# Kernel tuning notes

Measured on AMD Instinct MI355X. Metric: run time of the kernel, lower is better.

The kernel has to match this reference:

```python
import jax, jax.numpy as jnp
import numpy as np
import itertools

L, F, T = 16, 2, 2**19          # levels, features/level, hashmap size
BASE, SCALE = 16, 1.5           # base resolution, per-level scale
N = 524288                      # batch of sample points
PRIMES = np.array([1, 2654435761, 805459861, 3674653429], dtype=np.uint32)


def hash_encode(x, table):
    """Multi-resolution hash-grid encoding. x: [N,d] in [0,1); table: [L,T,F]."""
    n, d = x.shape
    corners = jnp.asarray(list(itertools.product([0, 1], repeat=d)), dtype=jnp.uint32)  # [C,d]
    primes = jnp.asarray(PRIMES[:d])
    is_hi = corners.astype(bool)[None]          # [1,C,d]
    outs = []
    for l in range(L):
        res = float(np.floor(BASE * SCALE**l))
        pos = x * res
        p0f = jnp.floor(pos)
        frac = pos - p0f                         # [N,d]
        p0 = p0f.astype(jnp.uint32)
        coords = p0[:, None, :] + corners[None]  # [N,C,d] uint32 (wraps)
        m = coords * primes                      # [N,C,d]
        h = m[..., 0]
        for j in range(1, d):
            h = h ^ m[..., j]
        idx = (h % np.uint32(T)).astype(jnp.int32)              # [N,C]
        w = jnp.where(is_hi, frac[:, None, :], 1.0 - frac[:, None, :]).prod(-1)  # [N,C]
        feat = table[l][idx]                                    # [N,C,F]
        outs.append(jnp.einsum('nc,ncf->nf', w, feat))
    return jnp.concatenate(outs, axis=-1)        # [N, L*F]


def mlp(h, w_in, w_hid, w_out):
    """tcnn-style bias-free MLP, ReLU hidden, linear output."""
    h = jax.nn.relu(h @ w_in)
    for i in range(w_hid.shape[0]):
        h = jax.nn.relu(h @ w_hid[i])
    return h @ w_out


def setup_inputs() -> dict:
    key = jax.random.key(0)
    ks = jax.random.split(key, 20)
    def w(k, shape):
        fan = shape[-2]
        return jax.random.normal(k, shape, jnp.float32) / np.sqrt(fan).astype(np.float32)
    return {
        'x': jax.random.uniform(ks[0], (N, 3), jnp.float32),
        't': jax.random.uniform(ks[1], (1,), jnp.float32),
        'skip_alpha': jax.random.uniform(ks[2], (1,), jnp.float32),
        'table_s': jax.random.normal(ks[3], (L, T, F), jnp.float32) * 1e-2,
        'ws_in': w(ks[4], (32, 64)),
        'ws_hid': w(ks[5], (3, 64, 64)),
        'ws_out': w(ks[6], (64, 64)),
        'table_d': jax.random.normal(ks[7], (L, T, F), jnp.float32) * 1e-2,
        'wd_in': w(ks[8], (32, 64)),
        'wd_hid': w(ks[9], (3, 64, 64)),
        'wd_out': w(ks[10], (64, 64)),
        'w1_in': w(ks[11], (128, 64)),
        'w1_hid': w(ks[12], (1, 64, 64)),
        'w1_out': w(ks[13], (64, 128)),
        'w2_in': w(ks[14], (128, 64)),
        'w2_hid': w(ks[15], (1, 64, 64)),
        'w2_out': w(ks[16], (64, 1)),
    }


def reference(x, t, skip_alpha, table_s, ws_in, ws_hid, ws_out,
              table_d, wd_in, wd_hid, wd_out,
              w1_in, w1_hid, w1_out, w2_in, w2_hid, w2_out):
    static_features = mlp(hash_encode(x, table_s), ws_in, ws_hid, ws_out)          # [N,64]
    t_col = jnp.broadcast_to(t, (x.shape[0], 1))
    x4 = jnp.concatenate([x, t_col], axis=1)                                        # [N,4]
    dynamic_features = mlp(hash_encode(x4, table_d), wd_in, wd_hid, wd_out)        # [N,64]
    features = jnp.concatenate([static_features, dynamic_features], axis=-1)       # [N,128]
    out1 = mlp(features, w1_in, w1_hid, w1_out)                                     # [N,128]
    blended = out1 * skip_alpha + (1.0 - skip_alpha) * features
    return mlp(blended, w2_in, w2_hid, w2_out)                                      # [N,1]
```

## Files before the change

### kernel.cpp

```cpp
#include <hip/hip_runtime.h>
#include <hip/hip_bf16.h>
#include <stdint.h>

#define LVLS 16
#define TSZ  524288
#define TMASK 0x7FFFFu
#define NPTS 524288
#define P1 2654435761u
#define P2 805459861u
#define P3 3674653429u

__constant__ float RES_TAB[16] = {
    16.f, 24.f, 36.f, 54.f, 81.f, 121.f, 182.f, 273.f,
    410.f, 615.f, 922.f, 1383.f, 2075.f, 3113.f, 4670.f, 7006.f};

using f16x8 = __attribute__((ext_vector_type(8))) _Float16;
using f32x4 = __attribute__((ext_vector_type(4))) float;

union PackF16 { uint32_t u; _Float16 h[2]; };

constexpr int PS = 72;

struct WPtrs { const float* p[11]; };

__global__ void k_weights(WPtrs wp, _Float16* __restrict__ dst) {
    int id = blockIdx.x * 256 + threadIdx.x;
    if (id >= 69632) return;
    const int OFF[16] = {0,2048,6144,10240,14336,18432,20480,24576,28672,
                         32768,36864,45056,49152,57344,65536,69632};
    const int KK[15]  = {32,64,64,64,64,32,64,64,64,64,128,64,64,128,64};
    const int NN[15]  = {64,64,64,64,64,64,64,64,64,64,64,64,128,64,64};
    const int PSEL[15]= {0,1,1,1,2,3,4,4,4,5,6,7,8,9,10};
    const int POFF[15]= {0,0,4096,8192,0,0,0,4096,8192,0,0,0,0,0,0};
    int m = 0;
    while (id >= OFF[m+1]) m++;
    int local = id - OFF[m];
    int j    = local & 7;
    int lane = (local >> 3) & 63;
    int blk  = local >> 9;
    int KC   = KK[m] >> 5;
    int ct   = blk / KC;
    int kc   = blk - ct * KC;
    int k    = kc*32 + ((lane>>4)<<3) + j;
    int n    = ct*16 + (lane & 15);
    const float* src = wp.p[PSEL[m]] + POFF[m];
    dst[id] = (_Float16)src[k * NN[m] + n];
}

__global__ void k_tables(const float* __restrict__ ts, const float* __restrict__ td,
                         const float* __restrict__ tptr, uint2* __restrict__ Tc) {
    int id = blockIdx.x * 256 + threadIdx.x;
    int l = id >> 19, i = id & TMASK;
    float2 sv = ((const float2*)ts)[id];
    float res = RES_TAB[l];
    float tv  = tptr[0];
    float pt  = tv * res;
    float fpt = floorf(pt);
    float ft  = pt - fpt;
    uint32_t ut = (uint32_t)(int)fpt;
    uint32_t h0 = (ut * P3) & TMASK;
    uint32_t h1 = ((ut + 1u) * P3) & TMASK;
    const float2* tdl = (const float2*)td + (size_t)l * TSZ;
    float2 a = tdl[i ^ h0];
    float2 b = tdl[i ^ h1];
    PackF16 o0, o1;
    o0.h[0] = (_Float16)sv.x; o0.h[1] = (_Float16)sv.y;
    o1.h[0] = (_Float16)((1.f - ft) * a.x + ft * b.x);
    o1.h[1] = (_Float16)((1.f - ft) * a.y + ft * b.y);
    Tc[id] = make_uint2(o0.u, o1.u);
}

__device__ __forceinline__ void enc_batch4(const float* __restrict__ x,
                                           const uint2* __restrict__ tcl, float res,
                                           uint32_t* __restrict__ es,
                                           uint32_t* __restrict__ ed, int pb) {
    float fr[4][3];
    uint2 v[4][8];
#pragma unroll
    for (int b = 0; b < 4; b++) {
        int p = pb + b * 65536;
        float px = x[p*3+0]*res, py = x[p*3+1]*res, pz = x[p*3+2]*res;
        float fx = floorf(px), fy = floorf(py), fz = floorf(pz);
        fr[b][0] = px-fx; fr[b][1] = py-fy; fr[b][2] = pz-fz;
        uint32_t ux = (uint32_t)(int)fx, uy = (uint32_t)(int)fy, uz = (uint32_t)(int)fz;
        uint32_t hx[2] = {ux, ux + 1u};
        uint32_t hy[2] = {uy * P1, (uy + 1u) * P1};
        uint32_t hz[2] = {uz * P2, (uz + 1u) * P2};
#pragma unroll
        for (int c = 0; c < 8; c++) {
            uint32_t idx = (hx[c&1] ^ hy[(c>>1)&1] ^ hz[c>>2]) & TMASK;
            v[b][c] = tcl[idx];
        }
    }
#pragma unroll
    for (int b = 0; b < 4; b++) {
        float wxa[2] = {1.f - fr[b][0], fr[b][0]};
        float wya[2] = {1.f - fr[b][1], fr[b][1]};
        float wza[2] = {1.f - fr[b][2], fr[b][2]};
        float sA0 = 0.f, sA1 = 0.f, sD0 = 0.f, sD1 = 0.f;
#pragma unroll
        for (int c = 0; c < 8; c++) {
            float w = wxa[c&1] * wya[(c>>1)&1] * wza[c>>2];
            PackF16 s, d; s.u = v[b][c].x; d.u = v[b][c].y;
            sA0 += w * (float)s.h[0]; sA1 += w * (float)s.h[1];
            sD0 += w * (float)d.h[0]; sD1 += w * (float)d.h[1];
        }
        PackF16 o;
        int p = pb + b * 65536;
        o.h[0] = (_Float16)sA0; o.h[1] = (_Float16)sA1; es[p] = o.u;
        o.h[0] = (_Float16)sD0; o.h[1] = (_Float16)sD1; ed[p] = o.u;
    }
}

__launch_bounds__(256, 4)
__global__ void k_encode(const float* __restrict__ x,
                         const uint2* __restrict__ Tc,
                         uint32_t* __restrict__ EncS, uint32_t* __restrict__ EncD) {
    int tid = threadIdx.x;
    int cls = blockIdx.x & 7;
    int gt  = (blockIdx.x >> 3) * 256 + tid;
#pragma unroll
    for (int u3 = 0; u3 < 3; u3++) {
        int u = cls * 3 + u3;
        int l = 4 + (u >> 1);
        int pb = (u & 1) * 262144 + gt;
        enc_batch4(x, Tc + (size_t)l * TSZ, RES_TAB[l],
                   EncS + (size_t)l * NPTS, EncD + (size_t)l * NPTS, pb);
    }
    {
        int l = cls >> 1;
        int pb = (cls & 1) * 262144 + gt;
        enc_batch4(x, Tc + (size_t)l * TSZ, RES_TAB[l],
                   EncS + (size_t)l * NPTS, EncD + (size_t)l * NPTS, pb);
    }
}

__device__ __forceinline__ void wait_lds() {
    asm volatile("s_waitcnt lgkmcnt(0)" ::: "memory");
}

template<int KC, bool RELU>
__device__ __forceinline__ void mm2(const f16x8 a[2][4], const f16x8* __restrict__ B,
                                    _Float16* dst, int m, int quad, int lane) {
#pragma unroll
    for (int ct = 0; ct < 4; ct++) {
        f32x4 acc0 = {0.f,0.f,0.f,0.f}, acc1 = {0.f,0.f,0.f,0.f};
#pragma unroll
        for (int kc = 0; kc < KC; kc++) {
            f16x8 b = B[(ct*KC+kc)*64 + lane];
            acc0 = __builtin_amdgcn_mfma_f32_16x16x32_f16(a[0][kc], b, acc0, 0, 0, 0);
            acc1 = __builtin_amdgcn_mfma_f32_16x16x32_f16(a[1][kc], b, acc1, 0, 0, 0);
        }
#pragma unroll
        for (int i = 0; i < 4; i++) {
            float v0 = acc0[i], v1 = acc1[i];
            if (RELU) { v0 = fmaxf(v0, 0.f); v1 = fmaxf(v1, 0.f); }
            dst[(0*16 + quad*4+i)*PS + ct*16 + m] = (_Float16)v0;
            dst[(1*16 + quad*4+i)*PS + ct*16 + m] = (_Float16)v1;
        }
    }
}

template<int KC>
__device__ __forceinline__ void mm2_keep(const f16x8 a[2][4], const f16x8* __restrict__ B,
                                         _Float16* dst, PackF16 P[2][8],
                                         int m, int quad, int lane) {
#pragma unroll
    for (int ct = 0; ct < 4; ct++) {
        f32x4 acc0 = {0.f,0.f,0.f,0.f}, acc1 = {0.f,0.f,0.f,0.f};
#pragma unroll
        for (int kc = 0; kc < KC; kc++) {
            f16x8 b = B[(ct*KC+kc)*64 + lane];
            acc0 = __builtin_amdgcn_mfma_f32_16x16x32_f16(a[0][kc], b, acc0, 0, 0, 0);
            acc1 = __builtin_amdgcn_mfma_f32_16x16x32_f16(a[1][kc], b, acc1, 0, 0, 0);
        }
#pragma unroll
        for (int ih = 0; ih < 2; ih++) {
            PackF16 p0, p1;
            p0.h[0] = (_Float16)acc0[ih*2+0]; p0.h[1] = (_Float16)acc0[ih*2+1];
            p1.h[0] = (_Float16)acc1[ih*2+0]; p1.h[1] = (_Float16)acc1[ih*2+1];
            P[0][ct*2+ih] = p0; P[1][ct*2+ih] = p1;
            dst[(0*16 + quad*4+ih*2+0)*PS + ct*16 + m] = p0.h[0];
            dst[(0*16 + quad*4+ih*2+1)*PS + ct*16 + m] = p0.h[1];
            dst[(1*16 + quad*4+ih*2+0)*PS + ct*16 + m] = p1.h[0];
            dst[(1*16 + quad*4+ih*2+1)*PS + ct*16 + m] = p1.h[1];
        }
    }
}

template<int KC>
__device__ __forceinline__ void read_a(const _Float16* buf, f16x8 a[2][4], int m, int quad) {
#pragma unroll
    for (int rt = 0; rt < 2; rt++)
#pragma unroll
        for (int kc = 0; kc < KC; kc++)
            a[rt][kc] = *(const f16x8*)(buf + (rt*16 + m)*PS + kc*32 + quad*8);
}

__device__ __forceinline__ void read_a128(const _Float16* Fs, const _Float16* Fd,
                                          f16x8 a[2][4], int m, int quad) {
#pragma unroll
    for (int rt = 0; rt < 2; rt++) {
#pragma unroll
        for (int kc = 0; kc < 2; kc++) {
            a[rt][kc]   = *(const f16x8*)(Fs + (rt*16 + m)*PS + kc*32 + quad*8);
            a[rt][kc+2] = *(const f16x8*)(Fd + (rt*16 + m)*PS + kc*32 + quad*8);
        }
    }
}

__device__ __forceinline__ void load_enc(const uint32_t* __restrict__ Enc,
                                         int pbase, int m, int quad, f16x8 a[2][4]) {
#pragma unroll
    for (int rt = 0; rt < 2; rt++) {
        union { uint32_t u[4]; f16x8 v; } cv;
        int p = pbase + rt*16 + m;
#pragma unroll
        for (int j = 0; j < 4; j++)
            cv.u[j] = Enc[(size_t)(quad*4 + j) * NPTS + p];
        a[rt][0] = cv.v;
    }
}

__launch_bounds__(256, 4)
__global__ void k_mlp(const uint32_t* __restrict__ EncS, const uint32_t* __restrict__ EncD,
                      const _Float16* __restrict__ Wfrag, const float* __restrict__ alphap,
                      const float* __restrict__ w2out, float* __restrict__ out) {
    __shared__ _Float16 FsB[4][32*PS];
    __shared__ _Float16 FdB[4][32*PS];
    int tid  = threadIdx.x;
    int wave = tid >> 6, lane = tid & 63;
    int m = lane & 15, quad = lane >> 4;
    int pbase = blockIdx.x * 128 + wave * 32;
    _Float16* Fs = FsB[wave];
    _Float16* Fd = FdB[wave];
    const f16x8* W8 = (const f16x8*)Wfrag;
    float alpha = alphap[0];

    f16x8 a[2][4];
    PackF16 sP[2][8], dP[2][8];

    load_enc(EncS, pbase, m, quad, a);
    mm2<1, true>(a, W8 + 0,    Fs, m, quad, lane); wait_lds();
    read_a<2>(Fs, a, m, quad);
    mm2<2, true>(a, W8 + 256,  Fs, m, quad, lane); wait_lds();
    read_a<2>(Fs, a, m, quad);
    mm2<2, true>(a, W8 + 768,  Fs, m, quad, lane); wait_lds();
    read_a<2>(Fs, a, m, quad);
    mm2<2, true>(a, W8 + 1280, Fs, m, quad, lane); wait_lds();
    read_a<2>(Fs, a, m, quad);
    mm2_keep<2>(a, W8 + 1792, Fs, sP, m, quad, lane);
    load_enc(EncD, pbase, m, quad, a);
    mm2<1, true>(a, W8 + 2304, Fd, m, quad, lane); wait_lds();
    read_a<2>(Fd, a, m, quad);
    mm2<2, true>(a, W8 + 2560, Fd, m, quad, lane); wait_lds();
    read_a<2>(Fd, a, m, quad);
    mm2<2, true>(a, W8 + 3072, Fd, m, quad, lane); wait_lds();
    read_a<2>(Fd, a, m, quad);
    mm2<2, true>(a, W8 + 3584, Fd, m, quad, lane); wait_lds();
    read_a<2>(Fd, a, m, quad);
    mm2_keep<2>(a, W8 + 4096, Fd, dP, m, quad, lane); wait_lds();
    read_a128(Fs, Fd, a, m, quad);
    mm2<4, true>(a, W8 + 4608, Fs, m, quad, lane); wait_lds();
    read_a<2>(Fs, a, m, quad);
    mm2<2, true>(a, W8 + 5632, Fs, m, quad, lane); wait_lds();
    read_a<2>(Fs, a, m, quad);
#pragma unroll
    for (int ct = 0; ct < 8; ct++) {
        f32x4 acc0 = {0.f,0.f,0.f,0.f}, acc1 = {0.f,0.f,0.f,0.f};
#pragma unroll
        for (int kc = 0; kc < 2; kc++) {
            f16x8 b = W8[6144 + (ct*2+kc)*64 + lane];
            acc0 = __builtin_amdgcn_mfma_f32_16x16x32_f16(a[0][kc], b, acc0, 0, 0, 0);
            acc1 = __builtin_amdgcn_mfma_f32_16x16x32_f16(a[1][kc], b, acc1, 0, 0, 0);
        }
        _Float16* tgt = (ct < 4) ? Fs : Fd;
        int col = (ct & 3) * 16 + m;
#pragma unroll
        for (int i = 0; i < 4; i++) {
            float f0 = (ct < 4) ? (float)sP[0][ct*2 + (i>>1)].h[i&1]
                                : (float)dP[0][(ct-4)*2 + (i>>1)].h[i&1];
            float f1 = (ct < 4) ? (float)sP[1][ct*2 + (i>>1)].h[i&1]
                                : (float)dP[1][(ct-4)*2 + (i>>1)].h[i&1];
            tgt[(0*16 + quad*4+i)*PS + col] = (_Float16)(alpha*acc0[i] + (1.f-alpha)*f0);
            tgt[(1*16 + quad*4+i)*PS + col] = (_Float16)(alpha*acc1[i] + (1.f-alpha)*f1);
        }
    }
    wait_lds();
    read_a128(Fs, Fd, a, m, quad);
    mm2<4, true>(a, W8 + 7168, Fs, m, quad, lane); wait_lds();
    read_a<2>(Fs, a, m, quad);
    float rsum0[4] = {0.f,0.f,0.f,0.f}, rsum1[4] = {0.f,0.f,0.f,0.f};
#pragma unroll
    for (int ct = 0; ct < 4; ct++) {
        f32x4 acc0 = {0.f,0.f,0.f,0.f}, acc1 = {0.f,0.f,0.f,0.f};
#pragma unroll
        for (int kc = 0; kc < 2; kc++) {
            f16x8 b = W8[8192 + (ct*2+kc)*64 + lane];
            acc0 = __builtin_amdgcn_mfma_f32_16x16x32_f16(a[0][kc], b, acc0, 0, 0, 0);
            acc1 = __builtin_amdgcn_mfma_f32_16x16x32_f16(a[1][kc], b, acc1, 0, 0, 0);
        }
        float wv = w2out[ct*16 + m];
#pragma unroll
        for (int i = 0; i < 4; i++) {
            rsum0[i] += fmaxf(acc0[i], 0.f) * wv;
            rsum1[i] += fmaxf(acc1[i], 0.f) * wv;
        }
    }
#pragma unroll
    for (int off = 1; off < 16; off <<= 1) {
#pragma unroll
        for (int i = 0; i < 4; i++) {
            rsum0[i] += __shfl_xor(rsum0[i], off, 64);
            rsum1[i] += __shfl_xor(rsum1[i], off, 64);
        }
    }
    if (m == 0) {
#pragma unroll
        for (int i = 0; i < 4; i++) {
            out[pbase + 0*16 + quad*4 + i] = rsum0[i];
            out[pbase + 1*16 + quad*4 + i] = rsum1[i];
        }
    }
}

extern "C" void kernel_launch(void* const* d_in, const int* in_sizes, int n_in,
                              void* d_out, int out_size, void* d_ws, size_t ws_size,
                              hipStream_t stream) {
    const float* x      = (const float*)d_in[0];
    const float* t      = (const float*)d_in[1];
    const float* alpha  = (const float*)d_in[2];
    const float* tab_s  = (const float*)d_in[3];
    const float* ws_in  = (const float*)d_in[4];
    const float* ws_hid = (const float*)d_in[5];
    const float* ws_out = (const float*)d_in[6];
    const float* tab_d  = (const float*)d_in[7];
    const float* wd_in  = (const float*)d_in[8];
    const float* wd_hid = (const float*)d_in[9];
    const float* wd_out = (const float*)d_in[10];
    const float* w1_in  = (const float*)d_in[11];
    const float* w1_hid = (const float*)d_in[12];
    const float* w1_out = (const float*)d_in[13];
    const float* w2_in  = (const float*)d_in[14];
    const float* w2_hid = (const float*)d_in[15];
    const float* w2_out = (const float*)d_in[16];
    float* out = (float*)d_out;

    char* ws = (char*)d_ws;
    _Float16* Wfrag = (_Float16*)ws;
    uint2*    Tc    = (uint2*)(ws + 139264);
    uint32_t* EncS  = (uint32_t*)(ws + 139264 + 67108864);
    uint32_t* EncD  = EncS + (size_t)LVLS * NPTS;
    size_t needed = 139264 + 67108864 + 2ull * 33554432ull;
    if (ws_size < needed) return;

    WPtrs wp;
    wp.p[0] = ws_in;  wp.p[1] = ws_hid; wp.p[2] = ws_out;
    wp.p[3] = wd_in;  wp.p[4] = wd_hid; wp.p[5] = wd_out;
    wp.p[6] = w1_in;  wp.p[7] = w1_hid; wp.p[8] = w1_out;
    wp.p[9] = w2_in;  wp.p[10] = w2_hid;

    k_weights<<<272,   256, 0, stream>>>(wp, Wfrag);
    k_tables <<<32768, 256, 0, stream>>>(tab_s, tab_d, t, Tc);
    k_encode <<<2048,  256, 0, stream>>>(x, Tc, EncS, EncD);
    k_mlp    <<<NPTS/128, 256, 0, stream>>>(EncS, EncD, Wfrag, alpha, w2_out, out);
}
```

Before: 619.9 us.

## Fuse weight and table prep kernels; reorder per-level encode schedule

Merges the weight-fragment conversion and the combined hash-table build into one k_build launch. Table blocks are ordered by level groups (0-3, 12-15, 4-11) so the build order roughly matches the order in which k_encode reads levels, with the aim of cache reuse. k_encode now processes one point at a time per level in non-unrolled loops instead of batches of four, and drops the occupancy hint in the launch bounds. The new block mapping rewrites levels 12-15 twice, which adds redundant work. Processing one point at a time also leaves fewer independent gathers in flight per thread.

Result: faster. 597.3 us (-3.6%).

```diff
diff --git a/kernel.cpp b/kernel.cpp
--- a/kernel.cpp
+++ b/kernel.cpp
@@ -23,115 +23,133 @@
 
 struct WPtrs { const float* p[11]; };
 
-__global__ void k_weights(WPtrs wp, _Float16* __restrict__ dst) {
-    int id = blockIdx.x * 256 + threadIdx.x;
-    if (id >= 69632) return;
-    const int OFF[16] = {0,2048,6144,10240,14336,18432,20480,24576,28672,
-                         32768,36864,45056,49152,57344,65536,69632};
-    const int KK[15]  = {32,64,64,64,64,32,64,64,64,64,128,64,64,128,64};
-    const int NN[15]  = {64,64,64,64,64,64,64,64,64,64,64,64,128,64,64};
-    const int PSEL[15]= {0,1,1,1,2,3,4,4,4,5,6,7,8,9,10};
-    const int POFF[15]= {0,0,4096,8192,0,0,0,4096,8192,0,0,0,0,0,0};
-    int m = 0;
-    while (id >= OFF[m+1]) m++;
-    int local = id - OFF[m];
-    int j    = local & 7;
-    int lane = (local >> 3) & 63;
-    int blk  = local >> 9;
-    int KC   = KK[m] >> 5;
-    int ct   = blk / KC;
-    int kc   = blk - ct * KC;
-    int k    = kc*32 + ((lane>>4)<<3) + j;
-    int n    = ct*16 + (lane & 15);
-    const float* src = wp.p[PSEL[m]] + POFF[m];
-    dst[id] = (_Float16)src[k * NN[m] + n];
-}
-
-__global__ void k_tables(const float* __restrict__ ts, const float* __restrict__ td,
-                         const float* __restrict__ tptr, uint2* __restrict__ Tc) {
-    int id = blockIdx.x * 256 + threadIdx.x;
-    int l = id >> 19, i = id & TMASK;
-    float2 sv = ((const float2*)ts)[id];
-    float res = RES_TAB[l];
-    float tv  = tptr[0];
-    float pt  = tv * res;
-    float fpt = floorf(pt);
-    float ft  = pt - fpt;
-    uint32_t ut = (uint32_t)(int)fpt;
-    uint32_t h0 = (ut * P3) & TMASK;
-    uint32_t h1 = ((ut + 1u) * P3) & TMASK;
-    const float2* tdl = (const float2*)td + (size_t)l * TSZ;
-    float2 a = tdl[i ^ h0];
-    float2 b = tdl[i ^ h1];
-    PackF16 o0, o1;
-    o0.h[0] = (_Float16)sv.x; o0.h[1] = (_Float16)sv.y;
-    o1.h[0] = (_Float16)((1.f - ft) * a.x + ft * b.x);
-    o1.h[1] = (_Float16)((1.f - ft) * a.y + ft * b.y);
-    Tc[id] = make_uint2(o0.u, o1.u);
-}
-
-__device__ __forceinline__ void enc_batch4(const float* __restrict__ x,
-                                           const uint2* __restrict__ tcl, float res,
-                                           uint32_t* __restrict__ es,
-                                           uint32_t* __restrict__ ed, int pb) {
-    float fr[4][3];
-    uint2 v[4][8];
-#pragma unroll
-    for (int b = 0; b < 4; b++) {
-        int p = pb + b * 65536;
-        float px = x[p*3+0]*res, py = x[p*3+1]*res, pz = x[p*3+2]*res;
-        float fx = floorf(px), fy = floorf(py), fz = floorf(pz);
-        fr[b][0] = px-fx; fr[b][1] = py-fy; fr[b][2] = pz-fz;
-        uint32_t ux = (uint32_t)(int)fx, uy = (uint32_t)(int)fy, uz = (uint32_t)(int)fz;
-        uint32_t hx[2] = {ux, ux + 1u};
-        uint32_t hy[2] = {uy * P1, (uy + 1u) * P1};
-        uint32_t hz[2] = {uz * P2, (uz + 1u) * P2};
-#pragma unroll
-        for (int c = 0; c < 8; c++) {
-            uint32_t idx = (hx[c&1] ^ hy[(c>>1)&1] ^ hz[c>>2]) & TMASK;
-            v[b][c] = tcl[idx];
-        }
-    }
-#pragma unroll
-    for (int b = 0; b < 4; b++) {
-        float wxa[2] = {1.f - fr[b][0], fr[b][0]};
-        float wya[2] = {1.f - fr[b][1], fr[b][1]};
-        float wza[2] = {1.f - fr[b][2], fr[b][2]};
-        float sA0 = 0.f, sA1 = 0.f, sD0 = 0.f, sD1 = 0.f;
-#pragma unroll
-        for (int c = 0; c < 8; c++) {
-            float w = wxa[c&1] * wya[(c>>1)&1] * wza[c>>2];
-            PackF16 s, d; s.u = v[b][c].x; d.u = v[b][c].y;
-            sA0 += w * (float)s.h[0]; sA1 += w * (float)s.h[1];
-            sD0 += w * (float)d.h[0]; sD1 += w * (float)d.h[1];
-        }
-        PackF16 o;
-        int p = pb + b * 65536;
-        o.h[0] = (_Float16)sA0; o.h[1] = (_Float16)sA1; es[p] = o.u;
-        o.h[0] = (_Float16)sD0; o.h[1] = (_Float16)sD1; ed[p] = o.u;
-    }
-}
-
-__launch_bounds__(256, 4)
+__global__ void k_build(const float* __restrict__ ts, const float* __restrict__ td,
+                        const float* __restrict__ tptr, uint2* __restrict__ Tc,
+                        WPtrs wp, _Float16* __restrict__ wdst) {
+    int B = blockIdx.x;
+    int tid = threadIdx.x;
+    if (B < 40960) {
+        int c = B & 7, j = B >> 3;
+        int l, i;
+        if (j < 1024) {
+            l = c >> 1;
+            i = (c & 1) * 262144 + j * 256 + tid;
+        } else if (j < 3072) {
+            l = 12 + (c >> 1);
+            i = (j - 1024) * 256 + tid;
+        } else {
+            l = 4 + c;
+            i = (j - 3072) * 256 + tid;
+        }
+        int id = l * TSZ + i;
+        float2 sv = ((const float2*)ts)[id];
+        float res = RES_TAB[l];
+        float tv  = tptr[0];
+        float pt  = tv * res;
+        float fpt = floorf(pt);
+        float ft  = pt - fpt;
+        uint32_t ut = (uint32_t)(int)fpt;
+        uint32_t h0 = (ut * P3) & TMASK;
+        uint32_t h1 = ((ut + 1u) * P3) & TMASK;
+        const float2* tdl = (const float2*)td + (size_t)l * TSZ;
+        float2 a = tdl[i ^ h0];
+        float2 b = tdl[i ^ h1];
+        PackF16 o0, o1;
+        o0.h[0] = (_Float16)sv.x; o0.h[1] = (_Float16)sv.y;
+        o1.h[0] = (_Float16)((1.f - ft) * a.x + ft * b.x);
+        o1.h[1] = (_Float16)((1.f - ft) * a.y + ft * b.y);
+        Tc[id] = make_uint2(o0.u, o1.u);
+    } else {
+        int id = (B - 40960) * 256 + tid;
+        if (id >= 69632) return;
+        const int OFF[16] = {0,2048,6144,10240,14336,18432,20480,24576,28672,
+                             32768,36864,45056,49152,57344,65536,69632};
+        const int KK[15]  = {32,64,64,64,64,32,64,64,64,64,128,64,64,128,64};
+        const int NN[15]  = {64,64,64,64,64,64,64,64,64,64,64,64,128,64,64};
+        const int PSEL[15]= {0,1,1,1,2,3,4,4,4,5,6,7,8,9,10};
+        const int POFF[15]= {0,0,4096,8192,0,0,0,4096,8192,0,0,0,0,0,0};
+        int m = 0;
+        while (id >= OFF[m+1]) m++;
+        int local = id - OFF[m];
+        int jj   = local & 7;
+        int lane = (local >> 3) & 63;
+        int blk  = local >> 9;
+        int KC   = KK[m] >> 5;
+        int ct   = blk / KC;
+        int kc   = blk - ct * KC;
+        int k    = kc*32 + ((lane>>4)<<3) + jj;
+        int n    = ct*16 + (lane & 15);
+        const float* src = wp.p[PSEL[m]] + POFF[m];
+        wdst[id] = (_Float16)src[k * NN[m] + n];
+    }
+}
+
+__device__ __forceinline__ void enc_point(const float* __restrict__ x,
+                                          const uint2* __restrict__ tcl, float res,
+                                          uint32_t* __restrict__ es,
+                                          uint32_t* __restrict__ ed, int p) {
+    float px = x[p*3+0]*res, py = x[p*3+1]*res, pz = x[p*3+2]*res;
+    float fx = floorf(px), fy = floorf(py), fz = floorf(pz);
+    float wx = px-fx, wy = py-fy, wz = pz-fz;
+    uint32_t ux = (uint32_t)(int)fx, uy = (uint32_t)(int)fy, uz = (uint32_t)(int)fz;
+    uint32_t hx[2] = {ux, ux + 1u};
+    uint32_t hy[2] = {uy * P1, (uy + 1u) * P1};
+    uint32_t hz[2] = {uz * P2, (uz + 1u) * P2};
+    uint2 v[8];
+#pragma unroll
+    for (int c = 0; c < 8; c++) {
+        uint32_t idx = (hx[c&1] ^ hy[(c>>1)&1] ^ hz[c>>2]) & TMASK;
+        v[c] = tcl[idx];
+    }
+    float wxa[2] = {1.f-wx, wx}, wya[2] = {1.f-wy, wy}, wza[2] = {1.f-wz, wz};
+    float sA0 = 0.f, sA1 = 0.f, sD0 = 0.f, sD1 = 0.f;
+#pragma unroll
+    for (int c = 0; c < 8; c++) {
+        float w = wxa[c&1] * wya[(c>>1)&1] * wza[c>>2];
+        PackF16 s, d; s.u = v[c].x; d.u = v[c].y;
+        sA0 += w * (float)s.h[0]; sA1 += w * (float)s.h[1];
+        sD0 += w * (float)d.h[0]; sD1 += w * (float)d.h[1];
+    }
+    PackF16 o;
+    o.h[0] = (_Float16)sA0; o.h[1] = (_Float16)sA1; es[p] = o.u;
+    o.h[0] = (_Float16)sD0; o.h[1] = (_Float16)sD1; ed[p] = o.u;
+}
+
+__launch_bounds__(256)
 __global__ void k_encode(const float* __restrict__ x,
                          const uint2* __restrict__ Tc,
                          uint32_t* __restrict__ EncS, uint32_t* __restrict__ EncD) {
     int tid = threadIdx.x;
-    int cls = blockIdx.x & 7;
+    int c   = blockIdx.x & 7;
     int gt  = (blockIdx.x >> 3) * 256 + tid;
-#pragma unroll
-    for (int u3 = 0; u3 < 3; u3++) {
-        int u = cls * 3 + u3;
-        int l = 4 + (u >> 1);
-        int pb = (u & 1) * 262144 + gt;
-        enc_batch4(x, Tc + (size_t)l * TSZ, RES_TAB[l],
-                   EncS + (size_t)l * NPTS, EncD + (size_t)l * NPTS, pb);
-    }
     {
-        int l = cls >> 1;
-        int pb = (cls & 1) * 262144 + gt;
-        enc_batch4(x, Tc + (size_t)l * TSZ, RES_TAB[l],
-                   EncS + (size_t)l * NPTS, EncD + (size_t)l * NPTS, pb);
+        int l = 4 + c;
+        const uint2* tcl = Tc + (size_t)l * TSZ;
+        uint32_t* es = EncS + (size_t)l * NPTS;
+        uint32_t* ed = EncD + (size_t)l * NPTS;
+        float res = RES_TAB[l];
+        for (int q = 0; q < 8; q++)
+            enc_point(x, tcl, res, es, ed, gt + q * 65536);
+    }
+    {
+        int l = 12 + (c >> 1);
+        const uint2* tcl = Tc + (size_t)l * TSZ;
+        uint32_t* es = EncS + (size_t)l * NPTS;
+        uint32_t* ed = EncD + (size_t)l * NPTS;
+        float res = RES_TAB[l];
+        int pb = (c & 1) * 262144 + gt;
+        for (int q = 0; q < 4; q++)
+            enc_point(x, tcl, res, es, ed, pb + q * 65536);
+    }
+    {
+        int l = c >> 1;
+        const uint2* tcl = Tc + (size_t)l * TSZ;
+        uint32_t* es = EncS + (size_t)l * NPTS;
+        uint32_t* ed = EncD + (size_t)l * NPTS;
+        float res = RES_TAB[l];
+        int pb = (c & 1) * 262144 + gt;
+        for (int q = 0; q < 4; q++)
+            enc_point(x, tcl, res, es, ed, pb + q * 65536);
     }
 }
 
@@ -360,8 +378,7 @@
     wp.p[6] = w1_in;  wp.p[7] = w1_hid; wp.p[8] = w1_out;
     wp.p[9] = w2_in;  wp.p[10] = w2_hid;
 
-    k_weights<<<272,   256, 0, stream>>>(wp, Wfrag);
-    k_tables <<<32768, 256, 0, stream>>>(tab_s, tab_d, t, Tc);
+    k_build  <<<41232, 256, 0, stream>>>(tab_s, tab_d, t, Tc, wp, Wfrag);
     k_encode <<<2048,  256, 0, stream>>>(x, Tc, EncS, EncD);
     k_mlp    <<<NPTS/128, 256, 0, stream>>>(EncS, EncD, Wfrag, alpha, w2_out, out);
 }
```
